# Kernel tuning notes

Measured on AMD Instinct MI355X. Metric: run time of the kernel, lower is better.

Reference implementation:

```python
import jax, jax.numpy as jnp
import numpy as np

S = 2048        # q_len == context_length
HID = 4096      # hidden_size
NH = 32         # num_attention_heads
NKV = 8         # num_key_value_heads
HD = HID // NH  # head_dim = 128
THETA = 10000.0


def setup_inputs() -> dict:
    key = jax.random.key(0)
    ks = jax.random.split(key, 5)
    hidden_states = jax.random.normal(ks[0], (1, S, HID), dtype=jnp.float32)
    # 1x1 Conv2d weights == linear weights (out_ch, in_ch)
    wq = jax.random.normal(ks[1], (NH * HD, HID), dtype=jnp.float32) * 0.02
    wk = jax.random.normal(ks[2], (NKV * HD, HID), dtype=jnp.float32) * 0.02
    wv = jax.random.normal(ks[3], (NKV * HD, HID), dtype=jnp.float32) * 0.02
    wo = jax.random.normal(ks[4], (HID, NH * HD), dtype=jnp.float32) * 0.02
    # RoPE tables: rotate() only ever uses the first half_dim of cos/sin,
    # so build (1,1,S,half) directly (equivalent to cat(freqs,freqs) then slice).
    half = HD // 2
    inv_freq = 1.0 / (THETA ** (jnp.arange(0, HD, 2, dtype=jnp.float32) / HD))
    freqs = jnp.outer(jnp.arange(S, dtype=jnp.float32), inv_freq)  # (S, half)
    cos = jnp.cos(freqs)[None, None]  # (1,1,S,half)
    sin = jnp.sin(freqs)[None, None]
    # additive causal mask (1,1,S,S): 0 on/below diagonal, large negative above
    causal_mask = jnp.where(
        jnp.arange(S)[:, None] >= jnp.arange(S)[None, :], 0.0, -1e9
    ).astype(jnp.float32)[None, None]
    return dict(hidden_states=hidden_states, wq=wq, wk=wk, wv=wv, wo=wo,
                cos=cos, sin=sin, causal_mask=causal_mask)


def _rope(x, cos, sin):
    # x: (H, S, D); cos/sin: (1,1,S,D/2)
    half = x.shape[-1] // 2
    x1, x2 = x[..., :half], x[..., half:]
    c, s = cos[0, 0], sin[0, 0]  # (S, half), broadcasts over heads
    return jnp.concatenate([x1 * c - x2 * s, x2 * c + x1 * s], axis=-1)


def reference(hidden_states, wq, wk, wv, wo, cos, sin, causal_mask):
    x = hidden_states[0]               # (S, HID); bsz hard-coded to 1 in source
    seq = x.shape[0]
    # 1x1 conv projections == matmul; channel layout is head-major (h*HD + d)
    q = (x @ wq.T).reshape(seq, NH, HD).transpose(1, 0, 2)    # (NH, S, D)
    k = (x @ wk.T).reshape(seq, NKV, HD).transpose(1, 0, 2)   # (NKV, S, D)
    v = (x @ wv.T).reshape(seq, NKV, HD).transpose(1, 0, 2)   # (NKV, S, D)
    q = _rope(q, cos, sin)
    k = _rope(k, cos, sin)
    # repeat_kv: unsqueeze(1).repeat(n_rep).view -> head idx = rep*NKV + kv == tile
    n_rep = NH // NKV
    k = jnp.tile(k, (n_rep, 1, 1))     # (NH, S, D)
    v = jnp.tile(v, (n_rep, 1, 1))
    scale = 1.0 / np.sqrt(HD).astype(np.float32)
    scores = jnp.einsum('hqd,hkd->hqk', q, k) * scale + causal_mask[0, 0]
    attn = jax.nn.softmax(scores, axis=-1)                    # == ANE_softmax
    out = jnp.einsum('hqk,hkd->hqd', attn, v)                 # (NH, S, D)
    out = out.transpose(1, 0, 2).reshape(seq, NH * HD)        # (S, HID)
    return (out @ wo.T)[None]                                 # (1, S, HID)
```

## Files before the change

### kernel.cpp

```cpp
#include <hip/hip_runtime.h>
#include <hip/hip_bf16.h>

#define S_LEN 2048
#define HID   4096
#define NH    32
#define NKV   8
#define HD    128
#define QKV_N 6144
#define KDIM  4096

typedef __attribute__((ext_vector_type(8))) short short8;
typedef __attribute__((ext_vector_type(4))) float floatx4;
typedef unsigned short ushort;

__device__ __forceinline__ unsigned short f2bu(float f) {
  __hip_bfloat16 b = __float2bfloat16(f);
  return *reinterpret_cast<unsigned short*>(&b);
}
__device__ __forceinline__ void store_c(float* p, float v) { *p = v; }
__device__ __forceinline__ void store_c(__hip_bfloat16* p, float v) { *p = __float2bfloat16(v); }

__device__ __forceinline__ void async_copy16(const void* g, void* l) {
  __builtin_amdgcn_global_load_lds((const __attribute__((address_space(1))) void*)g,
                                   (__attribute__((address_space(3))) void*)l, 16, 0, 0);
}

struct bf16x4 { __hip_bfloat16 a, b, c, d; };
__global__ void cvt_f32_bf16(const float* __restrict__ src, __hip_bfloat16* __restrict__ dst, int n4) {
  int i = blockIdx.x * blockDim.x + threadIdx.x;
  if (i < n4) {
    float4 v = ((const float4*)src)[i];
    bf16x4 o = { __float2bfloat16(v.x), __float2bfloat16(v.y),
                 __float2bfloat16(v.z), __float2bfloat16(v.w) };
    ((bf16x4*)dst)[i] = o;
  }
}

template <typename CT>
__global__ __launch_bounds__(256, 2) void gemm_nt(const __hip_bfloat16* __restrict__ A,
                                                  const __hip_bfloat16* __restrict__ B,
                                                  CT* __restrict__ C, int M, int N, int K) {
  __shared__ __align__(16) ushort As[128 * 64];
  __shared__ __align__(16) ushort Bs[128 * 64];
  const int tid  = threadIdx.x;
  const int bm   = blockIdx.y * 128;
  const int bn   = blockIdx.x * 128;
  const int wave = tid >> 6;
  const int lane = tid & 63;
  const int ww   = (wave >> 1) * 64;
  const int wc   = (wave & 1) * 64;
  const int l15  = lane & 15;
  const int quad = lane >> 4;

  const ushort* Au = (const ushort*)A;
  const ushort* Bu = (const ushort*)B;

  const int rr  = lane >> 3;
  const int cc  = lane & 7;
  const int gch = cc ^ rr;
  const ushort* Ag = Au + (size_t)(bm + wave * 32 + rr) * K + gch * 8;
  const ushort* Bg = Bu + (size_t)(bn + wave * 32 + rr) * K + gch * 8;

  floatx4 acc[4][4] = {};

  for (int k0 = 0; k0 < K; k0 += 64) {
    __syncthreads();
#pragma unroll
    for (int e = 0; e < 4; ++e) {
      async_copy16(Ag + (size_t)(e * 8) * K + k0, &As[(wave * 32 + e * 8) * 64]);
      async_copy16(Bg + (size_t)(e * 8) * K + k0, &Bs[(wave * 32 + e * 8) * 64]);
    }
    __syncthreads();
#pragma unroll
    for (int kd = 0; kd < 2; ++kd) {
      short8 af[4], bf[4];
#pragma unroll
      for (int i = 0; i < 4; ++i) {
        af[i] = *(const short8*)&As[(ww + i * 16 + l15) * 64 + ((kd * 4 + quad) ^ (l15 & 7)) * 8];
        bf[i] = *(const short8*)&Bs[(wc + i * 16 + l15) * 64 + ((kd * 4 + quad) ^ (l15 & 7)) * 8];
      }
#pragma unroll
      for (int mi = 0; mi < 4; ++mi)
#pragma unroll
        for (int ni = 0; ni < 4; ++ni)
          acc[mi][ni] = __builtin_amdgcn_mfma_f32_16x16x32_bf16(af[mi], bf[ni], acc[mi][ni], 0, 0, 0);
    }
  }
#pragma unroll
  for (int mi = 0; mi < 4; ++mi)
#pragma unroll
    for (int ni = 0; ni < 4; ++ni)
#pragma unroll
      for (int r = 0; r < 4; ++r) {
        int row = bm + ww + mi * 16 + quad * 4 + r;
        int col = bn + wc + ni * 16 + l15;
        store_c(&C[(size_t)row * N + col], acc[mi][ni][r]);
      }
}

__global__ void rope_qk(const __hip_bfloat16* __restrict__ QKV,
                        const float* __restrict__ cosp, const float* __restrict__ sinp,
                        __hip_bfloat16* __restrict__ Qh, __hip_bfloat16* __restrict__ Kh) {
  int s = blockIdx.y;
  int col = blockIdx.x * 256 + threadIdx.x;
  if (col >= 5120) return;
  const size_t base = (size_t)s * QKV_N;
  float x = __bfloat162float(QKV[base + col]);
  int dd = col & 127;
  float val;
  if (dd < 64) {
    float xp = __bfloat162float(QKV[base + col + 64]);
    val = x * cosp[s * 64 + dd] - xp * sinp[s * 64 + dd];
  } else {
    int f = dd - 64;
    float xp = __bfloat162float(QKV[base + col - 64]);
    val = x * cosp[s * 64 + f] + xp * sinp[s * 64 + f];
  }
  if (col < HID) {
    int h = col >> 7;
    Qh[((size_t)h * S_LEN + s) * HD + dd] = __float2bfloat16(val);
  } else {
    int h = (col - HID) >> 7;
    Kh[((size_t)h * S_LEN + s) * HD + dd] = __float2bfloat16(val);
  }
}

__global__ void v_transpose(const __hip_bfloat16* __restrict__ QKV, __hip_bfloat16* __restrict__ Vt) {
  __shared__ ushort tile[64][130];
  int h = blockIdx.y;
  int s0 = blockIdx.x * 64;
  int t = threadIdx.x;
  const ushort* src = (const ushort*)QKV;
#pragma unroll
  for (int i = 0; i < 32; ++i) {
    int flat = i * 256 + t;
    int r = flat >> 7, c = flat & 127;
    tile[r][c] = src[(size_t)(s0 + r) * QKV_N + 5120 + h * 128 + c];
  }
  __syncthreads();
  ushort* dst = (ushort*)Vt;
#pragma unroll
  for (int i = 0; i < 8; ++i) {
    int g = i * 256 + t;
    int d = g >> 4, j4 = (g & 15) * 4;
    ushort4 o;
    o.x = tile[j4][d]; o.y = tile[j4 + 1][d]; o.z = tile[j4 + 2][d]; o.w = tile[j4 + 3][d];
    *(ushort4*)&dst[((size_t)h * HD + d) * S_LEN + s0 + j4] = o;
  }
}

__global__ __launch_bounds__(256, 2) void attn(const __hip_bfloat16* __restrict__ Qh,
                                               const __hip_bfloat16* __restrict__ Kh,
                                               const __hip_bfloat16* __restrict__ Vt,
                                               __hip_bfloat16* __restrict__ AO) {
  __shared__ __align__(16) ushort Ks[2][64][128];
  __shared__ __align__(16) ushort P[4][32][72];
  const int bi   = blockIdx.x;
  const int head = bi & 31;
  const int slot = (bi >> 5) & 7;
  const int qt   = (bi >= 256) ? (2 * slot) : (15 - 2 * slot);
  const int wave = threadIdx.x >> 6;
  const int lane = threadIdx.x & 63;
  const int l15 = lane & 15, quad = lane >> 4;
  const int q0 = qt * 128 + wave * 32;
  const int hk = head & 7;
  const ushort* Qu = (const ushort*)Qh + (size_t)head * S_LEN * HD;
  const ushort* Ku = (const ushort*)Kh + (size_t)hk * S_LEN * HD;
  const ushort* Vu = (const ushort*)Vt + (size_t)hk * HD * S_LEN;

  const int rr4  = lane >> 4;
  const int cc16 = lane & 15;

  short8 qf[2][4];
#pragma unroll
  for (int mt = 0; mt < 2; ++mt)
#pragma unroll
    for (int kd = 0; kd < 4; ++kd)
      qf[mt][kd] = *(const short8*)(Qu + (size_t)(q0 + mt * 16 + l15) * HD + kd * 32 + quad * 8);

  floatx4 o[2][8] = {};
  float mst[2][4], lsum[2][4];
#pragma unroll
  for (int mt = 0; mt < 2; ++mt)
#pragma unroll
    for (int r = 0; r < 4; ++r) { mst[mt][r] = -1e30f; lsum[mt][r] = 0.f; }

  const float scale = 0.08838834764831845f;
  const int nsteps = 2 * (qt + 1);
  const int jendw = q0 + 32;

  auto stage = [&](int b, int j0) {
#pragma unroll
    for (int e = 0; e < 4; ++e) {
      int rt = e * 4 + rr4;
      int gc = cc16 ^ rt;
      async_copy16(Ku + (size_t)(j0 + wave * 16 + rt) * HD + gc * 8,
                   &Ks[b][wave * 16 + e * 4][0]);
    }
  };
  stage(0, 0);

  for (int s = 0; s < nsteps; ++s) {
    const int j0 = s * 64;
    __syncthreads();
    if (s + 1 < nsteps) stage((s + 1) & 1, (s + 1) * 64);
    if (j0 >= jendw) continue;
    const int b = s & 1;

    short8 vf0[8];
#pragma unroll
    for (int t = 0; t < 8; ++t)
      vf0[t] = *(const short8*)(Vu + (size_t)(t * 16 + l15) * S_LEN + j0 + quad * 8);

    floatx4 sc[2][4];
#pragma unroll
    for (int mt = 0; mt < 2; ++mt)
#pragma unroll
      for (int nt = 0; nt < 4; ++nt) sc[mt][nt] = floatx4{0.f, 0.f, 0.f, 0.f};
#pragma unroll
    for (int nt = 0; nt < 4; ++nt) {
      short8 kf[4];
#pragma unroll
      for (int kd = 0; kd < 4; ++kd)
        kf[kd] = *(const short8*)&Ks[b][nt * 16 + l15][((kd * 4 + quad) ^ l15) * 8];
#pragma unroll
      for (int mt = 0; mt < 2; ++mt)
#pragma unroll
        for (int kd = 0; kd < 4; ++kd)
          sc[mt][nt] = __builtin_amdgcn_mfma_f32_16x16x32_bf16(qf[mt][kd], kf[kd], sc[mt][nt], 0, 0, 0);
    }

    const bool domask = (j0 + 64 > q0);
#pragma unroll
    for (int mt = 0; mt < 2; ++mt)
#pragma unroll
      for (int r = 0; r < 4; ++r) {
        const int row = q0 + mt * 16 + quad * 4 + r;
        float v[4];
#pragma unroll
        for (int nt = 0; nt < 4; ++nt) {
          float x = sc[mt][nt][r] * scale;
          if (domask && (j0 + nt * 16 + l15 > row)) x = -1e30f;
          v[nt] = x;
        }
        float vm = fmaxf(fmaxf(v[0], v[1]), fmaxf(v[2], v[3]));
        vm = fmaxf(vm, __shfl_xor(vm, 1));
        vm = fmaxf(vm, __shfl_xor(vm, 2));
        vm = fmaxf(vm, __shfl_xor(vm, 4));
        vm = fmaxf(vm, __shfl_xor(vm, 8));
        const float mnew = fmaxf(mst[mt][r], vm);
        const float alpha = __expf(mst[mt][r] - mnew);
        float ps = 0.f;
#pragma unroll
        for (int nt = 0; nt < 4; ++nt) {
          float p = __expf(v[nt] - mnew);
          ps += p;
          P[wave][mt * 16 + quad * 4 + r][nt * 16 + l15] = f2bu(p);
        }
        ps += __shfl_xor(ps, 1);
        ps += __shfl_xor(ps, 2);
        ps += __shfl_xor(ps, 4);
        ps += __shfl_xor(ps, 8);
        lsum[mt][r] = lsum[mt][r] * alpha + ps;
        mst[mt][r] = mnew;
#pragma unroll
        for (int t = 0; t < 8; ++t) o[mt][t][r] *= alpha;
      }

    short8 vf1[8];
#pragma unroll
    for (int t = 0; t < 8; ++t)
      vf1[t] = *(const short8*)(Vu + (size_t)(t * 16 + l15) * S_LEN + j0 + 32 + quad * 8);

    asm volatile("s_waitcnt lgkmcnt(0)" ::: "memory");
    short8 pf[2][2];
#pragma unroll
    for (int mt = 0; mt < 2; ++mt)
#pragma unroll
      for (int hh = 0; hh < 2; ++hh)
        pf[mt][hh] = *(const short8*)&P[wave][mt * 16 + l15][hh * 32 + quad * 8];
#pragma unroll
    for (int t = 0; t < 8; ++t)
#pragma unroll
      for (int mt = 0; mt < 2; ++mt) {
        o[mt][t] = __builtin_amdgcn_mfma_f32_16x16x32_bf16(pf[mt][0], vf0[t], o[mt][t], 0, 0, 0);
        o[mt][t] = __builtin_amdgcn_mfma_f32_16x16x32_bf16(pf[mt][1], vf1[t], o[mt][t], 0, 0, 0);
      }
  }

#pragma unroll
  for (int mt = 0; mt < 2; ++mt)
#pragma unroll
    for (int r = 0; r < 4; ++r) {
      const int row = q0 + mt * 16 + quad * 4 + r;
      const float inv = 1.0f / lsum[mt][r];
#pragma unroll
      for (int t = 0; t < 8; ++t)
        AO[(size_t)row * HID + head * HD + t * 16 + l15] = __float2bfloat16(o[mt][t][r] * inv);
    }
}

extern "C" void kernel_launch(void* const* d_in, const int* in_sizes, int n_in,
                              void* d_out, int out_size, void* d_ws, size_t ws_size,
                              hipStream_t stream) {
  const float* x    = (const float*)d_in[0];
  const float* wq   = (const float*)d_in[1];
  const float* wk   = (const float*)d_in[2];
  const float* wv   = (const float*)d_in[3];
  const float* wo   = (const float*)d_in[4];
  const float* cosp = (const float*)d_in[5];
  const float* sinp = (const float*)d_in[6];
  float* out = (float*)d_out;

  char* ws = (char*)d_ws;
  size_t off = 0;
  auto alloc = [&](size_t bytes) { char* p = ws + off; off += (bytes + 255) & ~255ull; return p; };
  __hip_bfloat16* Xb   = (__hip_bfloat16*)alloc((size_t)S_LEN * KDIM * 2);
  __hip_bfloat16* Wqkv = (__hip_bfloat16*)alloc((size_t)QKV_N * KDIM * 2);
  __hip_bfloat16* Wob  = (__hip_bfloat16*)alloc((size_t)HID * HID * 2);
  __hip_bfloat16* QKVb = (__hip_bfloat16*)alloc((size_t)S_LEN * QKV_N * 2);
  __hip_bfloat16* Qh   = (__hip_bfloat16*)alloc((size_t)NH * S_LEN * HD * 2);
  __hip_bfloat16* Kh   = (__hip_bfloat16*)alloc((size_t)NKV * S_LEN * HD * 2);
  __hip_bfloat16* Vt   = (__hip_bfloat16*)alloc((size_t)NKV * HD * S_LEN * 2);
  __hip_bfloat16* AO   = (__hip_bfloat16*)alloc((size_t)S_LEN * HID * 2);

  auto cvt = [&](const float* s, __hip_bfloat16* dpt, size_t n) {
    int n4 = (int)(n / 4);
    cvt_f32_bf16<<<dim3((n4 + 255) / 256), dim3(256), 0, stream>>>(s, dpt, n4);
  };
  cvt(x, Xb, (size_t)S_LEN * KDIM);
  cvt(wq, Wqkv, (size_t)HID * KDIM);
  cvt(wk, Wqkv + (size_t)HID * KDIM, (size_t)NKV * HD * KDIM);
  cvt(wv, Wqkv + (size_t)(HID + NKV * HD) * KDIM, (size_t)NKV * HD * KDIM);
  cvt(wo, Wob, (size_t)HID * HID);

  gemm_nt<__hip_bfloat16><<<dim3(QKV_N / 128, S_LEN / 128), dim3(256), 0, stream>>>(
      Xb, Wqkv, QKVb, S_LEN, QKV_N, KDIM);
  rope_qk<<<dim3(20, S_LEN), dim3(256), 0, stream>>>(QKVb, cosp, sinp, Qh, Kh);
  v_transpose<<<dim3(S_LEN / 64, NKV), dim3(256), 0, stream>>>(QKVb, Vt);
  attn<<<dim3(512), dim3(256), 0, stream>>>(Qh, Kh, Vt, AO);
  gemm_nt<float><<<dim3(HID / 128, S_LEN / 128), dim3(256), 0, stream>>>(
      AO, Wob, out, S_LEN, HID, KDIM);
}
```

Measured before the change: 572.4 us.

## Shrink attention tiles to 64 query rows, 32-key blocks, higher occupancy

Restructures the attention kernel so each block handles 64 query rows (16 per wave) and steps over 32-key blocks, doubling the grid to 1024 blocks with launch bounds raised to 4 blocks per SM. The old paired-tile load balancing is replaced by a longest-first ordering. Softmax switches to exp2 with a pre-folded log2e scale. The O rescale is skipped when no row max changed, and the row-sum reduction is deferred to the end. This aims to improve occupancy, load balance and softmax cost. In exchange each wave does less MFMA work per K/V load, so V is reloaded from global more often and synchronisation per step rises.

```diff
diff --git a/kernel.cpp b/kernel.cpp
--- a/kernel.cpp
+++ b/kernel.cpp
@@ -149,20 +149,19 @@
   }
 }
 
-__global__ __launch_bounds__(256, 2) void attn(const __hip_bfloat16* __restrict__ Qh,
+__global__ __launch_bounds__(256, 4) void attn(const __hip_bfloat16* __restrict__ Qh,
                                                const __hip_bfloat16* __restrict__ Kh,
                                                const __hip_bfloat16* __restrict__ Vt,
                                                __hip_bfloat16* __restrict__ AO) {
-  __shared__ __align__(16) ushort Ks[2][64][128];
-  __shared__ __align__(16) ushort P[4][32][72];
+  __shared__ __align__(16) ushort Ks[2][32][128];
+  __shared__ __align__(16) ushort P[4][16][40];
   const int bi   = blockIdx.x;
   const int head = bi & 31;
-  const int slot = (bi >> 5) & 7;
-  const int qt   = (bi >= 256) ? (2 * slot) : (15 - 2 * slot);
+  const int tile = 31 - ((bi >> 5) & 31);
   const int wave = threadIdx.x >> 6;
   const int lane = threadIdx.x & 63;
   const int l15 = lane & 15, quad = lane >> 4;
-  const int q0 = qt * 128 + wave * 32;
+  const int q0 = tile * 64 + wave * 16;
   const int hk = head & 7;
   const ushort* Qu = (const ushort*)Qh + (size_t)head * S_LEN * HD;
   const ushort* Ku = (const ushort*)Kh + (size_t)hk * S_LEN * HD;
@@ -171,133 +170,128 @@
   const int rr4  = lane >> 4;
   const int cc16 = lane & 15;
 
-  short8 qf[2][4];
-#pragma unroll
-  for (int mt = 0; mt < 2; ++mt)
-#pragma unroll
-    for (int kd = 0; kd < 4; ++kd)
-      qf[mt][kd] = *(const short8*)(Qu + (size_t)(q0 + mt * 16 + l15) * HD + kd * 32 + quad * 8);
-
-  floatx4 o[2][8] = {};
-  float mst[2][4], lsum[2][4];
-#pragma unroll
-  for (int mt = 0; mt < 2; ++mt)
-#pragma unroll
-    for (int r = 0; r < 4; ++r) { mst[mt][r] = -1e30f; lsum[mt][r] = 0.f; }
-
-  const float scale = 0.08838834764831845f;
-  const int nsteps = 2 * (qt + 1);
-  const int jendw = q0 + 32;
+  short8 qf[4];
+#pragma unroll
+  for (int kd = 0; kd < 4; ++kd)
+    qf[kd] = *(const short8*)(Qu + (size_t)(q0 + l15) * HD + kd * 32 + quad * 8);
+
+  floatx4 o[8] = {};
+  float mst[4], lsum[4];
+#pragma unroll
+  for (int r = 0; r < 4; ++r) { mst[r] = -1e30f; lsum[r] = 0.f; }
+
+  const float c2 = 0.08838834764831845f * 1.4426950408889634f;
+  const int nsteps = 2 * tile + 2;
+  const int jendw = q0 + 16;
 
   auto stage = [&](int b, int j0) {
 #pragma unroll
-    for (int e = 0; e < 4; ++e) {
+    for (int e = 0; e < 2; ++e) {
       int rt = e * 4 + rr4;
-      int gc = cc16 ^ rt;
-      async_copy16(Ku + (size_t)(j0 + wave * 16 + rt) * HD + gc * 8,
-                   &Ks[b][wave * 16 + e * 4][0]);
+      int row = wave * 8 + rt;
+      int gc = cc16 ^ (row & 15);
+      async_copy16(Ku + (size_t)(j0 + row) * HD + gc * 8, &Ks[b][wave * 8 + e * 4][0]);
     }
   };
   stage(0, 0);
 
   for (int s = 0; s < nsteps; ++s) {
-    const int j0 = s * 64;
+    const int j0 = s * 32;
     __syncthreads();
-    if (s + 1 < nsteps) stage((s + 1) & 1, (s + 1) * 64);
+    if (s + 1 < nsteps) stage((s + 1) & 1, j0 + 32);
     if (j0 >= jendw) continue;
     const int b = s & 1;
 
-    short8 vf0[8];
-#pragma unroll
-    for (int t = 0; t < 8; ++t)
-      vf0[t] = *(const short8*)(Vu + (size_t)(t * 16 + l15) * S_LEN + j0 + quad * 8);
-
-    floatx4 sc[2][4];
-#pragma unroll
-    for (int mt = 0; mt < 2; ++mt)
-#pragma unroll
-      for (int nt = 0; nt < 4; ++nt) sc[mt][nt] = floatx4{0.f, 0.f, 0.f, 0.f};
-#pragma unroll
-    for (int nt = 0; nt < 4; ++nt) {
+    short8 vfa[4];
+#pragma unroll
+    for (int t = 0; t < 4; ++t)
+      vfa[t] = *(const short8*)(Vu + (size_t)(t * 16 + l15) * S_LEN + j0 + quad * 8);
+
+    floatx4 sc[2];
+#pragma unroll
+    for (int nt = 0; nt < 2; ++nt) {
+      sc[nt] = floatx4{0.f, 0.f, 0.f, 0.f};
       short8 kf[4];
 #pragma unroll
       for (int kd = 0; kd < 4; ++kd)
         kf[kd] = *(const short8*)&Ks[b][nt * 16 + l15][((kd * 4 + quad) ^ l15) * 8];
 #pragma unroll
-      for (int mt = 0; mt < 2; ++mt)
-#pragma unroll
-        for (int kd = 0; kd < 4; ++kd)
-          sc[mt][nt] = __builtin_amdgcn_mfma_f32_16x16x32_bf16(qf[mt][kd], kf[kd], sc[mt][nt], 0, 0, 0);
-    }
-
-    const bool domask = (j0 + 64 > q0);
-#pragma unroll
-    for (int mt = 0; mt < 2; ++mt)
+      for (int kd = 0; kd < 4; ++kd)
+        sc[nt] = __builtin_amdgcn_mfma_f32_16x16x32_bf16(qf[kd], kf[kd], sc[nt], 0, 0, 0);
+    }
+
+    const bool domask = (j0 + 32 > q0);
+    float v0[4], v1[4], mnew[4];
+    bool ch = false;
+#pragma unroll
+    for (int r = 0; r < 4; ++r) {
+      const int row = q0 + quad * 4 + r;
+      float a = sc[0][r] * c2;
+      float bb = sc[1][r] * c2;
+      if (domask) {
+        if (j0 + l15 > row) a = -1e30f;
+        if (j0 + 16 + l15 > row) bb = -1e30f;
+      }
+      v0[r] = a; v1[r] = bb;
+      float vm = fmaxf(a, bb);
+      vm = fmaxf(vm, __shfl_xor(vm, 1));
+      vm = fmaxf(vm, __shfl_xor(vm, 2));
+      vm = fmaxf(vm, __shfl_xor(vm, 4));
+      vm = fmaxf(vm, __shfl_xor(vm, 8));
+      mnew[r] = fmaxf(mst[r], vm);
+      ch |= (mnew[r] > mst[r]);
+    }
+    float psr[4];
+#pragma unroll
+    for (int r = 0; r < 4; ++r) {
+      float p0 = exp2f(v0[r] - mnew[r]);
+      float p1 = exp2f(v1[r] - mnew[r]);
+      P[wave][quad * 4 + r][l15] = f2bu(p0);
+      P[wave][quad * 4 + r][16 + l15] = f2bu(p1);
+      psr[r] = p0 + p1;
+    }
+    if (__ballot(ch)) {
 #pragma unroll
       for (int r = 0; r < 4; ++r) {
-        const int row = q0 + mt * 16 + quad * 4 + r;
-        float v[4];
-#pragma unroll
-        for (int nt = 0; nt < 4; ++nt) {
-          float x = sc[mt][nt][r] * scale;
-          if (domask && (j0 + nt * 16 + l15 > row)) x = -1e30f;
-          v[nt] = x;
-        }
-        float vm = fmaxf(fmaxf(v[0], v[1]), fmaxf(v[2], v[3]));
-        vm = fmaxf(vm, __shfl_xor(vm, 1));
-        vm = fmaxf(vm, __shfl_xor(vm, 2));
-        vm = fmaxf(vm, __shfl_xor(vm, 4));
-        vm = fmaxf(vm, __shfl_xor(vm, 8));
-        const float mnew = fmaxf(mst[mt][r], vm);
-        const float alpha = __expf(mst[mt][r] - mnew);
-        float ps = 0.f;
-#pragma unroll
-        for (int nt = 0; nt < 4; ++nt) {
-          float p = __expf(v[nt] - mnew);
-          ps += p;
-          P[wave][mt * 16 + quad * 4 + r][nt * 16 + l15] = f2bu(p);
-        }
-        ps += __shfl_xor(ps, 1);
-        ps += __shfl_xor(ps, 2);
-        ps += __shfl_xor(ps, 4);
-        ps += __shfl_xor(ps, 8);
-        lsum[mt][r] = lsum[mt][r] * alpha + ps;
-        mst[mt][r] = mnew;
-#pragma unroll
-        for (int t = 0; t < 8; ++t) o[mt][t][r] *= alpha;
+        float alpha = exp2f(mst[r] - mnew[r]);
+        lsum[r] = lsum[r] * alpha + psr[r];
+        mst[r] = mnew[r];
+#pragma unroll
+        for (int t = 0; t < 8; ++t) o[t][r] *= alpha;
       }
-
-    short8 vf1[8];
+    } else {
+#pragma unroll
+      for (int r = 0; r < 4; ++r) lsum[r] += psr[r];
+    }
+
+    short8 vfb[4];
+#pragma unroll
+    for (int t = 0; t < 4; ++t)
+      vfb[t] = *(const short8*)(Vu + (size_t)((t + 4) * 16 + l15) * S_LEN + j0 + quad * 8);
+
+    asm volatile("s_waitcnt lgkmcnt(0)" ::: "memory");
+    short8 pf = *(const short8*)&P[wave][l15][quad * 8];
+#pragma unroll
+    for (int t = 0; t < 4; ++t)
+      o[t] = __builtin_amdgcn_mfma_f32_16x16x32_bf16(pf, vfa[t], o[t], 0, 0, 0);
+#pragma unroll
+    for (int t = 0; t < 4; ++t)
+      o[t + 4] = __builtin_amdgcn_mfma_f32_16x16x32_bf16(pf, vfb[t], o[t + 4], 0, 0, 0);
+  }
+
+#pragma unroll
+  for (int r = 0; r < 4; ++r) {
+    float ls = lsum[r];
+    ls += __shfl_xor(ls, 1);
+    ls += __shfl_xor(ls, 2);
+    ls += __shfl_xor(ls, 4);
+    ls += __shfl_xor(ls, 8);
+    const float inv = 1.0f / ls;
+    const int row = q0 + quad * 4 + r;
 #pragma unroll
     for (int t = 0; t < 8; ++t)
-      vf1[t] = *(const short8*)(Vu + (size_t)(t * 16 + l15) * S_LEN + j0 + 32 + quad * 8);
-
-    asm volatile("s_waitcnt lgkmcnt(0)" ::: "memory");
-    short8 pf[2][2];
-#pragma unroll
-    for (int mt = 0; mt < 2; ++mt)
-#pragma unroll
-      for (int hh = 0; hh < 2; ++hh)
-        pf[mt][hh] = *(const short8*)&P[wave][mt * 16 + l15][hh * 32 + quad * 8];
-#pragma unroll
-    for (int t = 0; t < 8; ++t)
-#pragma unroll
-      for (int mt = 0; mt < 2; ++mt) {
-        o[mt][t] = __builtin_amdgcn_mfma_f32_16x16x32_bf16(pf[mt][0], vf0[t], o[mt][t], 0, 0, 0);
-        o[mt][t] = __builtin_amdgcn_mfma_f32_16x16x32_bf16(pf[mt][1], vf1[t], o[mt][t], 0, 0, 0);
-      }
-  }
-
-#pragma unroll
-  for (int mt = 0; mt < 2; ++mt)
-#pragma unroll
-    for (int r = 0; r < 4; ++r) {
-      const int row = q0 + mt * 16 + quad * 4 + r;
-      const float inv = 1.0f / lsum[mt][r];
-#pragma unroll
-      for (int t = 0; t < 8; ++t)
-        AO[(size_t)row * HID + head * HD + t * 16 + l15] = __float2bfloat16(o[mt][t][r] * inv);
-    }
+      AO[(size_t)row * HID + head * HD + t * 16 + l15] = __float2bfloat16(o[t][r] * inv);
+  }
 }
 
 extern "C" void kernel_launch(void* const* d_in, const int* in_sizes, int n_in,
@@ -338,7 +332,7 @@
       Xb, Wqkv, QKVb, S_LEN, QKV_N, KDIM);
   rope_qk<<<dim3(20, S_LEN), dim3(256), 0, stream>>>(QKVb, cosp, sinp, Qh, Kh);
   v_transpose<<<dim3(S_LEN / 64, NKV), dim3(256), 0, stream>>>(QKVb, Vt);
-  attn<<<dim3(512), dim3(256), 0, stream>>>(Qh, Kh, Vt, AO);
+  attn<<<dim3(1024), dim3(256), 0, stream>>>(Qh, Kh, Vt, AO);
   gemm_nt<float><<<dim3(HID / 128, S_LEN / 128), dim3(256), 0, stream>>>(
       AO, Wob, out, S_LEN, HID, KDIM);
 }
```

Result: slower. 609.2 us (+6.4%).
